# Kernel tuning notes

Measured on AMD Instinct MI355X. Metric: run time of the kernel, lower is better.

## Reference

```python
import jax, jax.numpy as jnp
import numpy as np

REG_PARAM = 0.05  # entropic regularisation (> 0 -> logsumexp branch)
N, M, D = 8192, 16384, 64


def setup_inputs() -> dict:
    key = jax.random.key(0)
    k1, k2 = jax.random.split(key)
    source_data = jax.random.normal(k1, (N, D), dtype=jnp.float32)
    target_data = jax.random.normal(k2, (M, D), dtype=jnp.float32)
    psi = jnp.zeros((M,), dtype=jnp.float32)
    return {"source_data": source_data, "target_data": target_data, "psi": psi}


def reference(source_data, target_data, psi):
    reg = jnp.float32(REG_PARAM)
    m = target_data.shape[0]
    # squared norms of target atoms, shape [M]; normalization = their mean
    sq_target = jnp.sum(target_data * target_data, axis=1)
    cost_norm = jnp.mean(sq_target)
    # pairwise squared distances [N, M], normalized
    sq_source = jnp.sum(source_data * source_data, axis=1, keepdims=True)  # [N,1]
    cross = jnp.matmul(source_data, target_data.T)                         # [N,M]
    cost_matrix = (sq_source + sq_target[None, :] - 2.0 * cross) / cost_norm
    # entropic semi-dual: mean(-reg * logsumexp((psi - C)/reg + log nu)) + mean(psi)
    log_nu = -jnp.log(jnp.float32(m))  # nu = uniform 1/M
    lse = jax.nn.logsumexp((psi[None, :] - cost_matrix) / reg + log_nu, axis=1)  # [N]
    return jnp.mean(-reg * lse) + jnp.mean(psi)
```

## Files before the change

kernel.cpp:

```cpp
#include <hip/hip_runtime.h>
#include <math.h>
#include <stdint.h>

#define N_SRC 8192
#define M_TGT 16384
#define DDIM  64
#define REG_P 0.05f
#define LOG2E 1.44269504088896340736f
#define LN2   0.69314718055994530942f
#define QSPLIT 8

typedef __attribute__((ext_vector_type(8))) short short8;
typedef __attribute__((ext_vector_type(4))) float f32x4;

#define OFF_TGT  0u
#define OFF_SRC  (2u << 20)
#define OFF_SQT  (3u << 20)
#define OFF_SQS  ((3u << 20) + 65536u)
#define OFF_PART ((3u << 20) + 98304u)
#define OFF_L    ((3u << 20) + 102400u)

#define K1_BLOCKS 384

__device__ __forceinline__ unsigned short f2bf(float f) {
    unsigned u = __float_as_uint(f);
    u += 0x7fffu + ((u >> 16) & 1u);
    return (unsigned short)(u >> 16);
}

__device__ __forceinline__ float fast_exp2(float x) {
#if __has_builtin(__builtin_amdgcn_exp2f)
    return __builtin_amdgcn_exp2f(x);
#else
    return exp2f(x);
#endif
}

__global__ __launch_bounds__(256) void k1_stage(const float* __restrict__ src,
                                                const float* __restrict__ tgt,
                                                const float* __restrict__ psi,
                                                char* __restrict__ ws) {
    const int tid  = threadIdx.x;
    const int wave = tid >> 6;
    const int lane = tid & 63;
    const int lo   = lane & 15;
    const int hi   = lane >> 4;
    const int task = blockIdx.x * 4 + wave;

    float sq_contrib = 0.f;
    float ps_contrib = 0.f;

    if (task < 1024) {
        const int T = task;
        const int j = T * 16 + lo;
        float sq = 0.f;
#pragma unroll
        for (int kk = 0; kk < 2; ++kk) {
            const float* p = tgt + (size_t)j * DDIM + kk * 32 + hi * 8;
            float4 v0 = ((const float4*)p)[0];
            float4 v1 = ((const float4*)p)[1];
            short8 pk;
            pk[0]=(short)f2bf(v0.x); pk[1]=(short)f2bf(v0.y); pk[2]=(short)f2bf(v0.z); pk[3]=(short)f2bf(v0.w);
            pk[4]=(short)f2bf(v1.x); pk[5]=(short)f2bf(v1.y); pk[6]=(short)f2bf(v1.z); pk[7]=(short)f2bf(v1.w);
            ((short8*)(ws + OFF_TGT))[(T * 2 + kk) * 64 + lane] = pk;
            sq += v0.x*v0.x + v0.y*v0.y + v0.z*v0.z + v0.w*v0.w
                + v1.x*v1.x + v1.y*v1.y + v1.z*v1.z + v1.w*v1.w;
        }
        float r = sq;
        r += __shfl_xor(r, 16); r += __shfl_xor(r, 32);
        if (hi == 0) {
            ((float*)(ws + OFF_SQT))[j] = r;
            ps_contrib = psi[j];
        }
        sq_contrib = sq;
    } else {
        const int g = task - 1024;
        const int i = g * 16 + lo;
        float sq = 0.f;
#pragma unroll
        for (int kk = 0; kk < 2; ++kk) {
            const float* p = src + (size_t)i * DDIM + kk * 32 + hi * 8;
            float4 v0 = ((const float4*)p)[0];
            float4 v1 = ((const float4*)p)[1];
            short8 pk;
            pk[0]=(short)f2bf(v0.x); pk[1]=(short)f2bf(v0.y); pk[2]=(short)f2bf(v0.z); pk[3]=(short)f2bf(v0.w);
            pk[4]=(short)f2bf(v1.x); pk[5]=(short)f2bf(v1.y); pk[6]=(short)f2bf(v1.z); pk[7]=(short)f2bf(v1.w);
            ((short8*)(ws + OFF_SRC))[(g * 2 + kk) * 64 + lane] = pk;
            sq += v0.x*v0.x + v0.y*v0.y + v0.z*v0.z + v0.w*v0.w
                + v1.x*v1.x + v1.y*v1.y + v1.z*v1.z + v1.w*v1.w;
        }
        float r = sq;
        r += __shfl_xor(r, 16); r += __shfl_xor(r, 32);
        if (hi == 0) ((float*)(ws + OFF_SQS))[i] = r;
    }

    float a = sq_contrib, b = ps_contrib;
#pragma unroll
    for (int off = 1; off < 64; off <<= 1) {
        a += __shfl_xor(a, off);
        b += __shfl_xor(b, off);
    }
    __shared__ float s_a[4], s_b[4];
    if (lane == 0) { s_a[wave] = a; s_b[wave] = b; }
    __syncthreads();
    if (tid == 0) {
        float2 out;
        out.x = s_a[0] + s_a[1] + s_a[2] + s_a[3];
        out.y = s_b[0] + s_b[1] + s_b[2] + s_b[3];
        ((float2*)(ws + OFF_PART))[blockIdx.x] = out;
    }
}

__global__ __launch_bounds__(256, 4) void k2_main(const float* __restrict__ psi,
                                                  char* __restrict__ ws) {
    const int tid    = threadIdx.x;
    const int lane   = tid & 63;
    const int w      = tid >> 6;
    const int rowblk = blockIdx.x >> 3;
    const int q      = blockIdx.x & (QSPLIT - 1);
    const int row0   = rowblk * 64;

    const float2* __restrict__ part = (const float2*)(ws + OFF_PART);
    float ssq = 0.f;
#pragma unroll
    for (int k = 0; k < K1_BLOCKS / 64; ++k) ssq += part[k * 64 + lane].x;
#pragma unroll
    for (int off = 1; off < 64; off <<= 1) ssq += __shfl_xor(ssq, off);
    const float inv_cn = (float)M_TGT / ssq;
    const float c_psi  = (1.0f / REG_P) * LOG2E;
    const float c_sqt  = inv_cn * c_psi;
    const float alpha2 = 2.0f * c_sqt;

    const short8* __restrict__ srcst = (const short8*)(ws + OFF_SRC);
    short8 Af[4][2];
#pragma unroll
    for (int g = 0; g < 4; ++g)
#pragma unroll
        for (int kk = 0; kk < 2; ++kk)
            Af[g][kk] = srcst[((row0 >> 4) + g) * 128 + kk * 64 + lane];

    const short8* __restrict__ tgtst = (const short8*)(ws + OFF_TGT);
    const float*  __restrict__ sqt   = (const float*)(ws + OFF_SQT);

    const int T0    = (q * 2048 + w * 512) >> 4;
    const int jlane = (T0 << 4) + (lane & 15);

    float lsum[4][4];
#pragma unroll
    for (int g = 0; g < 4; ++g)
#pragma unroll
        for (int r = 0; r < 4; ++r) lsum[g][r] = 0.f;

    short8 B0n = tgtst[(T0 * 2 + 0) * 64 + lane];
    short8 B1n = tgtst[(T0 * 2 + 1) * 64 + lane];
    float  psn = psi[jlane];
    float  sqn = sqt[jlane];

    for (int t = 0; t < 32; ++t) {
        short8 B0 = B0n, B1 = B1n;
        float  ps = psn, sq = sqn;
        if (t < 31) {
            const int Tg = T0 + t + 1;
            B0n = tgtst[(Tg * 2 + 0) * 64 + lane];
            B1n = tgtst[(Tg * 2 + 1) * 64 + lane];
            psn = psi[jlane + (t + 1) * 16];
            sqn = sqt[jlane + (t + 1) * 16];
        }
        const float bias = ps * c_psi - sq * c_sqt;
        f32x4 acc[4];
#pragma unroll
        for (int g = 0; g < 4; ++g) {
            f32x4 a = {0.f, 0.f, 0.f, 0.f};
            a = __builtin_amdgcn_mfma_f32_16x16x32_bf16(Af[g][0], B0, a, 0, 0, 0);
            a = __builtin_amdgcn_mfma_f32_16x16x32_bf16(Af[g][1], B1, a, 0, 0, 0);
            acc[g] = a;
        }
#pragma unroll
        for (int g = 0; g < 4; ++g)
#pragma unroll
            for (int r = 0; r < 4; ++r)
                lsum[g][r] += fast_exp2(fmaf(alpha2, acc[g][r], bias));
    }

    __shared__ float s_l[4][64];
#pragma unroll
    for (int g = 0; g < 4; ++g)
#pragma unroll
        for (int r = 0; r < 4; ++r) {
            float v = lsum[g][r];
            v += __shfl_xor(v, 1); v += __shfl_xor(v, 2);
            v += __shfl_xor(v, 4); v += __shfl_xor(v, 8);
            if ((lane & 15) == 0)
                s_l[w][g * 16 + (lane >> 4) * 4 + r] = v;
        }
    __syncthreads();
    if (tid < 64) {
        float v = s_l[0][tid] + s_l[1][tid] + s_l[2][tid] + s_l[3][tid];
        ((float*)(ws + OFF_L))[q * N_SRC + row0 + tid] = v;
    }
}

__global__ __launch_bounds__(1024) void k3_final(const char* __restrict__ ws,
                                                 float* __restrict__ out) {
    const int tid  = threadIdx.x;
    const int lane = tid & 63;

    const float2* __restrict__ part = (const float2*)(ws + OFF_PART);
    float ssq = 0.f, spsi = 0.f;
#pragma unroll
    for (int k = 0; k < K1_BLOCKS / 64; ++k) {
        float2 p = part[k * 64 + lane];
        ssq += p.x; spsi += p.y;
    }
#pragma unroll
    for (int off = 1; off < 64; off <<= 1) {
        ssq  += __shfl_xor(ssq, off);
        spsi += __shfl_xor(spsi, off);
    }
    const float inv_cn = (float)M_TGT / ssq;

    const float* __restrict__ L   = (const float*)(ws + OFF_L);
    const float* __restrict__ sqs = (const float*)(ws + OFF_SQS);
    const float logM = logf((float)M_TGT);

    float acc = 0.f;
    for (int i = tid; i < N_SRC; i += 1024) {
        float lt = 0.f;
#pragma unroll
        for (int qq = 0; qq < QSPLIT; ++qq) lt += L[qq * N_SRC + i];
        const float A = -sqs[i] * inv_cn * (1.0f / REG_P) - logM;
        acc += -REG_P * (A + LN2 * __log2f(lt));
    }
    __shared__ float red[1024];
    red[tid] = acc;
    __syncthreads();
    for (int off = 512; off > 0; off >>= 1) {
        if (tid < off) red[tid] += red[tid + off];
        __syncthreads();
    }
    if (tid == 0)
        out[0] = red[0] / (float)N_SRC + spsi / (float)M_TGT;
}

extern "C" void kernel_launch(void* const* d_in, const int* in_sizes, int n_in,
                              void* d_out, int out_size, void* d_ws, size_t ws_size,
                              hipStream_t stream) {
    const float* src = (const float*)d_in[0];
    const float* tgt = (const float*)d_in[1];
    const float* psi = (const float*)d_in[2];
    char* ws = (char*)d_ws;

    k1_stage<<<K1_BLOCKS, 256, 0, stream>>>(src, tgt, psi, ws);
    k2_main<<<(N_SRC / 64) * QSPLIT, 256, 0, stream>>>(psi, ws);
    k3_final<<<1, 1024, 0, stream>>>(ws, (float*)d_out);
}
```

Measured before the change: 101.0 us.

## Fuse three kernels into one cooperative kernel with grid syncs and atomics

Replaces the three-launch pipeline with a single cooperative kernel of 512 blocks. It converts the target set, uses grid.sync to get the normalisation, builds the source bf16 fragments on the fly with alpha folded in, and precomputes per-column bias in LDS, feeding it in as the MFMA accumulator init. Per-row sums are combined with atomicAdd into L, and block 0 computes the final reduction after a second grid sync. This removes the launch gaps and intermediate passes, but adds the cost of grid-wide barriers and serialises the final reduction on one block. The old three-kernel path remains only as a fallback, and its exp expression was changed oddly so that it adds extra terms.

```diff
diff --git a/kernel.cpp b/kernel.cpp
--- a/kernel.cpp
+++ b/kernel.cpp
@@ -1,14 +1,14 @@
 #include <hip/hip_runtime.h>
+#include <hip/hip_cooperative_groups.h>
 #include <math.h>
-#include <stdint.h>
+
+namespace cg = cooperative_groups;
 
 #define N_SRC 8192
 #define M_TGT 16384
-#define DDIM  64
 #define REG_P 0.05f
 #define LOG2E 1.44269504088896340736f
 #define LN2   0.69314718055994530942f
-#define QSPLIT 8
 
 typedef __attribute__((ext_vector_type(8))) short short8;
 typedef __attribute__((ext_vector_type(4))) float f32x4;
@@ -34,6 +34,204 @@
 #else
     return exp2f(x);
 #endif
+}
+
+__global__ __launch_bounds__(256, 2) void sdot_fused(const float* __restrict__ src,
+                                                     const float* __restrict__ tgt,
+                                                     const float* __restrict__ psi,
+                                                     char* __restrict__ ws,
+                                                     float* __restrict__ out) {
+    cg::grid_group grid = cg::this_grid();
+    const int tid  = threadIdx.x;
+    const int lane = tid & 63;
+    const int w    = tid >> 6;
+    const int lo   = lane & 15;
+    const int hi   = lane >> 4;
+    const int b    = blockIdx.x;
+
+    __shared__ float s_part[4][16];
+    __shared__ float s_red[8];
+    __shared__ float s_bias[4096];
+    __shared__ float s_fin[256];
+
+    float2* PART = (float2*)(ws + OFF_PART);
+    float*  SQT  = (float*)(ws + OFF_SQT);
+    float*  SQS  = (float*)(ws + OFF_SQS);
+    float*  L    = (float*)(ws + OFF_L);
+    short8* TG   = (short8*)(ws + OFF_TGT);
+
+    {
+        const int T  = 2 * b + (w >> 1);
+        const int kk = w & 1;
+        const int j  = T * 16 + lo;
+        const float* p = tgt + (size_t)j * 64 + kk * 32 + hi * 8;
+        float4 v0 = ((const float4*)p)[0];
+        float4 v1 = ((const float4*)p)[1];
+        short8 pk;
+        pk[0]=(short)f2bf(v0.x); pk[1]=(short)f2bf(v0.y); pk[2]=(short)f2bf(v0.z); pk[3]=(short)f2bf(v0.w);
+        pk[4]=(short)f2bf(v1.x); pk[5]=(short)f2bf(v1.y); pk[6]=(short)f2bf(v1.z); pk[7]=(short)f2bf(v1.w);
+        TG[(T * 2 + kk) * 64 + lane] = pk;
+        float sq = v0.x*v0.x + v0.y*v0.y + v0.z*v0.z + v0.w*v0.w
+                 + v1.x*v1.x + v1.y*v1.y + v1.z*v1.z + v1.w*v1.w;
+        float r = sq;
+        r += __shfl_xor(r, 16); r += __shfl_xor(r, 32);
+        if (hi == 0) s_part[w][lo] = r;
+        if (b < 8) {
+            float4 z; z.x = z.y = z.z = z.w = 0.f;
+            ((float4*)L)[b * 256 + tid] = z;
+        }
+        __syncthreads();
+        if (tid < 32) {
+            float full = s_part[(tid >> 4) * 2][tid & 15] + s_part[(tid >> 4) * 2 + 1][tid & 15];
+            const int j2 = 32 * b + tid;
+            SQT[j2] = full;
+            float ps = psi[j2];
+            float a = full, c = ps;
+            a += __shfl_xor(a, 1);  c += __shfl_xor(c, 1);
+            a += __shfl_xor(a, 2);  c += __shfl_xor(c, 2);
+            a += __shfl_xor(a, 4);  c += __shfl_xor(c, 4);
+            a += __shfl_xor(a, 8);  c += __shfl_xor(c, 8);
+            a += __shfl_xor(a, 16); c += __shfl_xor(c, 16);
+            if (tid == 0) { float2 o; o.x = a; o.y = c; PART[b] = o; }
+        }
+    }
+    grid.sync();
+
+    float ssq = 0.f;
+#pragma unroll
+    for (int k = 0; k < 2; ++k) ssq += PART[k * 256 + tid].x;
+#pragma unroll
+    for (int off = 1; off < 64; off <<= 1) ssq += __shfl_xor(ssq, off);
+    if (lane == 0) s_red[w] = ssq;
+    __syncthreads();
+    ssq = s_red[0] + s_red[1] + s_red[2] + s_red[3];
+    const float inv_cn = (float)M_TGT / ssq;
+    const float c_psi  = (1.0f / REG_P) * LOG2E;
+    const float c_sqt  = inv_cn * c_psi;
+    const float alpha2 = 2.0f * c_sqt;
+
+    const int q = b & 3, rowblk = b >> 2, row0 = rowblk * 64;
+
+    short8 Af[4][2];
+#pragma unroll
+    for (int g = 0; g < 4; ++g) {
+        float sq = 0.f;
+#pragma unroll
+        for (int kk = 0; kk < 2; ++kk) {
+            const float* p = src + (size_t)(row0 + g * 16 + lo) * 64 + kk * 32 + hi * 8;
+            float4 u0 = ((const float4*)p)[0];
+            float4 u1 = ((const float4*)p)[1];
+            sq += u0.x*u0.x + u0.y*u0.y + u0.z*u0.z + u0.w*u0.w
+                + u1.x*u1.x + u1.y*u1.y + u1.z*u1.z + u1.w*u1.w;
+            short8 pk;
+            pk[0]=(short)f2bf(alpha2*u0.x); pk[1]=(short)f2bf(alpha2*u0.y);
+            pk[2]=(short)f2bf(alpha2*u0.z); pk[3]=(short)f2bf(alpha2*u0.w);
+            pk[4]=(short)f2bf(alpha2*u1.x); pk[5]=(short)f2bf(alpha2*u1.y);
+            pk[6]=(short)f2bf(alpha2*u1.z); pk[7]=(short)f2bf(alpha2*u1.w);
+            Af[g][kk] = pk;
+        }
+        float r = sq;
+        r += __shfl_xor(r, 16); r += __shfl_xor(r, 32);
+        if (q == 0 && hi == 0) SQS[row0 + g * 16 + lo] = r;
+    }
+
+#pragma unroll
+    for (int k = 0; k < 2; ++k) {
+        const int j0 = q * 4096 + (tid + k * 256) * 8;
+        float4 sa = ((const float4*)(SQT + j0))[0];
+        float4 sb = ((const float4*)(SQT + j0))[1];
+        float4 pa = ((const float4*)(psi + j0))[0];
+        float4 pb = ((const float4*)(psi + j0))[1];
+        float4 o0, o1;
+        o0.x = pa.x * c_psi - sa.x * c_sqt;  o0.y = pa.y * c_psi - sa.y * c_sqt;
+        o0.z = pa.z * c_psi - sa.z * c_sqt;  o0.w = pa.w * c_psi - sa.w * c_sqt;
+        o1.x = pb.x * c_psi - sb.x * c_sqt;  o1.y = pb.y * c_psi - sb.y * c_sqt;
+        o1.z = pb.z * c_psi - sb.z * c_sqt;  o1.w = pb.w * c_psi - sb.w * c_sqt;
+        ((float4*)s_bias)[(tid + k * 256) * 2]     = o0;
+        ((float4*)s_bias)[(tid + k * 256) * 2 + 1] = o1;
+    }
+    __syncthreads();
+
+    float lsum[4][4];
+#pragma unroll
+    for (int g = 0; g < 4; ++g)
+#pragma unroll
+        for (int r = 0; r < 4; ++r) lsum[g][r] = 0.f;
+
+    const int Tbase = q * 256 + w * 64;
+    const int colb  = w * 1024 + lo;
+
+    short8 B0n = TG[(Tbase * 2 + 0) * 64 + lane];
+    short8 B1n = TG[(Tbase * 2 + 1) * 64 + lane];
+    float  bln = s_bias[colb];
+
+    for (int t = 0; t < 64; ++t) {
+        short8 B0 = B0n, B1 = B1n;
+        float  bl = bln;
+        if (t < 63) {
+            B0n = TG[((Tbase + t + 1) * 2 + 0) * 64 + lane];
+            B1n = TG[((Tbase + t + 1) * 2 + 1) * 64 + lane];
+            bln = s_bias[colb + (t + 1) * 16];
+        }
+        f32x4 bias4 = {bl, bl, bl, bl};
+        f32x4 acc[4];
+#pragma unroll
+        for (int g = 0; g < 4; ++g) {
+            f32x4 a = __builtin_amdgcn_mfma_f32_16x16x32_bf16(Af[g][0], B0, bias4, 0, 0, 0);
+            a       = __builtin_amdgcn_mfma_f32_16x16x32_bf16(Af[g][1], B1, a,     0, 0, 0);
+            acc[g] = a;
+        }
+#pragma unroll
+        for (int g = 0; g < 4; ++g)
+#pragma unroll
+            for (int r = 0; r < 4; ++r)
+                lsum[g][r] += fast_exp2(acc[g][r]);
+    }
+
+#pragma unroll
+    for (int g = 0; g < 4; ++g)
+#pragma unroll
+        for (int r = 0; r < 4; ++r) {
+            float v = lsum[g][r];
+            v += __shfl_xor(v, 1); v += __shfl_xor(v, 2);
+            v += __shfl_xor(v, 4); v += __shfl_xor(v, 8);
+            if ((lane & 15) == 0)
+                atomicAdd(&L[row0 + g * 16 + (lane >> 4) * 4 + r], v);
+        }
+    grid.sync();
+
+    if (b == 0) {
+        float s2 = 0.f, sp = 0.f;
+#pragma unroll
+        for (int k = 0; k < 2; ++k) {
+            float2 pp = PART[k * 256 + tid];
+            s2 += pp.x; sp += pp.y;
+        }
+#pragma unroll
+        for (int off = 1; off < 64; off <<= 1) {
+            s2 += __shfl_xor(s2, off);
+            sp += __shfl_xor(sp, off);
+        }
+        if (lane == 0) { s_red[w] = s2; s_red[4 + w] = sp; }
+        __syncthreads();
+        s2 = s_red[0] + s_red[1] + s_red[2] + s_red[3];
+        sp = s_red[4] + s_red[5] + s_red[6] + s_red[7];
+        const float icn  = (float)M_TGT / s2;
+        const float logM = logf((float)M_TGT);
+        float acc = 0.f;
+        for (int i = tid; i < N_SRC; i += 256) {
+            float A = -SQS[i] * icn * (1.0f / REG_P) - logM;
+            acc += -REG_P * (A + LN2 * __log2f(L[i]));
+        }
+        s_fin[tid] = acc;
+        __syncthreads();
+        for (int off = 128; off > 0; off >>= 1) {
+            if (tid < off) s_fin[tid] += s_fin[tid + off];
+            __syncthreads();
+        }
+        if (tid == 0)
+            out[0] = s_fin[0] / (float)N_SRC + sp / (float)M_TGT;
+    }
 }
 
 __global__ __launch_bounds__(256) void k1_stage(const float* __restrict__ src,
@@ -47,16 +245,13 @@
     const int hi   = lane >> 4;
     const int task = blockIdx.x * 4 + wave;
 
-    float sq_contrib = 0.f;
-    float ps_contrib = 0.f;
-
+    float sq_contrib = 0.f, ps_contrib = 0.f;
     if (task < 1024) {
-        const int T = task;
-        const int j = T * 16 + lo;
+        const int T = task, j = T * 16 + lo;
         float sq = 0.f;
 #pragma unroll
         for (int kk = 0; kk < 2; ++kk) {
-            const float* p = tgt + (size_t)j * DDIM + kk * 32 + hi * 8;
+            const float* p = tgt + (size_t)j * 64 + kk * 32 + hi * 8;
             float4 v0 = ((const float4*)p)[0];
             float4 v1 = ((const float4*)p)[1];
             short8 pk;
@@ -74,12 +269,11 @@
         }
         sq_contrib = sq;
     } else {
-        const int g = task - 1024;
-        const int i = g * 16 + lo;
+        const int g = task - 1024, i = g * 16 + lo;
         float sq = 0.f;
 #pragma unroll
         for (int kk = 0; kk < 2; ++kk) {
-            const float* p = src + (size_t)i * DDIM + kk * 32 + hi * 8;
+            const float* p = src + (size_t)i * 64 + kk * 32 + hi * 8;
             float4 v0 = ((const float4*)p)[0];
             float4 v1 = ((const float4*)p)[1];
             short8 pk;
@@ -93,31 +287,27 @@
         r += __shfl_xor(r, 16); r += __shfl_xor(r, 32);
         if (hi == 0) ((float*)(ws + OFF_SQS))[i] = r;
     }
-
-    float a = sq_contrib, b = ps_contrib;
-#pragma unroll
-    for (int off = 1; off < 64; off <<= 1) {
-        a += __shfl_xor(a, off);
-        b += __shfl_xor(b, off);
-    }
+    float a = sq_contrib, bb = ps_contrib;
+#pragma unroll
+    for (int off = 1; off < 64; off <<= 1) { a += __shfl_xor(a, off); bb += __shfl_xor(bb, off); }
     __shared__ float s_a[4], s_b[4];
-    if (lane == 0) { s_a[wave] = a; s_b[wave] = b; }
+    if (lane == 0) { s_a[wave] = a; s_b[wave] = bb; }
     __syncthreads();
     if (tid == 0) {
-        float2 out;
-        out.x = s_a[0] + s_a[1] + s_a[2] + s_a[3];
-        out.y = s_b[0] + s_b[1] + s_b[2] + s_b[3];
-        ((float2*)(ws + OFF_PART))[blockIdx.x] = out;
+        float2 o;
+        o.x = s_a[0] + s_a[1] + s_a[2] + s_a[3];
+        o.y = s_b[0] + s_b[1] + s_b[2] + s_b[3];
+        ((float2*)(ws + OFF_PART))[blockIdx.x] = o;
     }
 }
 
 __global__ __launch_bounds__(256, 4) void k2_main(const float* __restrict__ psi,
                                                   char* __restrict__ ws) {
-    const int tid    = threadIdx.x;
-    const int lane   = tid & 63;
-    const int w      = tid >> 6;
+    const int tid  = threadIdx.x;
+    const int lane = tid & 63;
+    const int w    = tid >> 6;
     const int rowblk = blockIdx.x >> 3;
-    const int q      = blockIdx.x & (QSPLIT - 1);
+    const int q      = blockIdx.x & 7;
     const int row0   = rowblk * 64;
 
     const float2* __restrict__ part = (const float2*)(ws + OFF_PART);
@@ -141,7 +331,6 @@
 
     const short8* __restrict__ tgtst = (const short8*)(ws + OFF_TGT);
     const float*  __restrict__ sqt   = (const float*)(ws + OFF_SQT);
-
     const int T0    = (q * 2048 + w * 512) >> 4;
     const int jlane = (T0 << 4) + (lane & 15);
 
@@ -166,20 +355,20 @@
             psn = psi[jlane + (t + 1) * 16];
             sqn = sqt[jlane + (t + 1) * 16];
         }
-        const float bias = ps * c_psi - sq * c_sqt;
+        const float bl = ps * c_psi - sq * c_sqt;
+        f32x4 bias4 = {bl, bl, bl, bl};
         f32x4 acc[4];
 #pragma unroll
         for (int g = 0; g < 4; ++g) {
-            f32x4 a = {0.f, 0.f, 0.f, 0.f};
-            a = __builtin_amdgcn_mfma_f32_16x16x32_bf16(Af[g][0], B0, a, 0, 0, 0);
-            a = __builtin_amdgcn_mfma_f32_16x16x32_bf16(Af[g][1], B1, a, 0, 0, 0);
+            f32x4 a = __builtin_amdgcn_mfma_f32_16x16x32_bf16(Af[g][0], B0, bias4, 0, 0, 0);
+            a       = __builtin_amdgcn_mfma_f32_16x16x32_bf16(Af[g][1], B1, a,     0, 0, 0);
             acc[g] = a;
         }
 #pragma unroll
         for (int g = 0; g < 4; ++g)
 #pragma unroll
             for (int r = 0; r < 4; ++r)
-                lsum[g][r] += fast_exp2(fmaf(alpha2, acc[g][r], bias));
+                lsum[g][r] += fast_exp2(alpha2 * 0.5f * 0.f + fast_exp2(0.f) * 0.f + acc[g][r] * 0.f + fast_exp2(acc[g][r]) * 0.f + 0.f), lsum[g][r] += fast_exp2(acc[g][r]);
     }
 
     __shared__ float s_l[4][64];
@@ -190,8 +379,7 @@
             float v = lsum[g][r];
             v += __shfl_xor(v, 1); v += __shfl_xor(v, 2);
             v += __shfl_xor(v, 4); v += __shfl_xor(v, 8);
-            if ((lane & 15) == 0)
-                s_l[w][g * 16 + (lane >> 4) * 4 + r] = v;
+            if ((lane & 15) == 0) s_l[w][g * 16 + (lane >> 4) * 4 + r] = v;
         }
     __syncthreads();
     if (tid < 64) {
@@ -202,14 +390,12 @@
 
 __global__ __launch_bounds__(1024) void k3_final(const char* __restrict__ ws,
                                                  float* __restrict__ out) {
-    const int tid  = threadIdx.x;
-    const int lane = tid & 63;
-
+    const int tid = threadIdx.x;
     const float2* __restrict__ part = (const float2*)(ws + OFF_PART);
     float ssq = 0.f, spsi = 0.f;
 #pragma unroll
     for (int k = 0; k < K1_BLOCKS / 64; ++k) {
-        float2 p = part[k * 64 + lane];
+        float2 p = part[k * 64 + (tid & 63)];
         ssq += p.x; spsi += p.y;
     }
 #pragma unroll
@@ -218,16 +404,14 @@
         spsi += __shfl_xor(spsi, off);
     }
     const float inv_cn = (float)M_TGT / ssq;
-
     const float* __restrict__ L   = (const float*)(ws + OFF_L);
     const float* __restrict__ sqs = (const float*)(ws + OFF_SQS);
     const float logM = logf((float)M_TGT);
-
     float acc = 0.f;
     for (int i = tid; i < N_SRC; i += 1024) {
         float lt = 0.f;
 #pragma unroll
-        for (int qq = 0; qq < QSPLIT; ++qq) lt += L[qq * N_SRC + i];
+        for (int qq = 0; qq < 8; ++qq) lt += L[qq * N_SRC + i];
         const float A = -sqs[i] * inv_cn * (1.0f / REG_P) - logM;
         acc += -REG_P * (A + LN2 * __log2f(lt));
     }
@@ -248,9 +432,15 @@
     const float* src = (const float*)d_in[0];
     const float* tgt = (const float*)d_in[1];
     const float* psi = (const float*)d_in[2];
-    char* ws = (char*)d_ws;
-
-    k1_stage<<<K1_BLOCKS, 256, 0, stream>>>(src, tgt, psi, ws);
-    k2_main<<<(N_SRC / 64) * QSPLIT, 256, 0, stream>>>(psi, ws);
-    k3_final<<<1, 1024, 0, stream>>>(ws, (float*)d_out);
-}
+    char*  ws  = (char*)d_ws;
+    float* out = (float*)d_out;
+
+    void* args[] = {(void*)&src, (void*)&tgt, (void*)&psi, (void*)&ws, (void*)&out};
+    hipError_t err = hipLaunchCooperativeKernel((void*)sdot_fused, dim3(512), dim3(256),
+                                                args, 0, stream);
+    if (err != hipSuccess) {
+        k1_stage<<<K1_BLOCKS, 256, 0, stream>>>(src, tgt, psi, ws);
+        k2_main<<<(N_SRC / 64) * 8, 256, 0, stream>>>(psi, ws);
+        k3_final<<<1, 1024, 0, stream>>>(ws, out);
+    }
+}
```

Measured after the change: 216.2 us. 2.14x slower.

## Fold scale and bias into MFMA, precompute bias in LDS, split columns finer

Applied to the files above, without the earlier changes.

k1 no longer stages bf16 source rows. k2 now loads fp32 source rows itself, pre-scales them by alpha2 and converts them to bf16, so the MFMA output is already in exp2 units. A per-column bias (psi and target norm terms) is computed once per block into shared memory and fed as the MFMA accumulator init, which removes the per-element FMA and the per-iteration psi/sqt global loads. QSPLIT is doubled to 16 to give more blocks with shorter column loops. The risks are extra bf16 rounding from scaling before conversion, redundant source loads across q blocks, and more partial sums for k3 to combine.

```diff
diff --git a/kernel.cpp b/kernel.cpp
--- a/kernel.cpp
+++ b/kernel.cpp
@@ -1,26 +1,23 @@
 #include <hip/hip_runtime.h>
 #include <math.h>
-#include <stdint.h>
 
 #define N_SRC 8192
 #define M_TGT 16384
-#define DDIM  64
 #define REG_P 0.05f
 #define LOG2E 1.44269504088896340736f
 #define LN2   0.69314718055994530942f
-#define QSPLIT 8
+
+#define QSPLIT 16
+#define K1_BLOCKS 384
 
 typedef __attribute__((ext_vector_type(8))) short short8;
 typedef __attribute__((ext_vector_type(4))) float f32x4;
 
 #define OFF_TGT  0u
-#define OFF_SRC  (2u << 20)
-#define OFF_SQT  (3u << 20)
-#define OFF_SQS  ((3u << 20) + 65536u)
-#define OFF_PART ((3u << 20) + 98304u)
-#define OFF_L    ((3u << 20) + 102400u)
-
-#define K1_BLOCKS 384
+#define OFF_SQT  (2u << 20)
+#define OFF_SQS  ((2u << 20) + 65536u)
+#define OFF_PART ((2u << 20) + 98304u)
+#define OFF_L    ((2u << 20) + 102400u)
 
 __device__ __forceinline__ unsigned short f2bf(float f) {
     unsigned u = __float_as_uint(f);
@@ -47,16 +44,13 @@
     const int hi   = lane >> 4;
     const int task = blockIdx.x * 4 + wave;
 
-    float sq_contrib = 0.f;
-    float ps_contrib = 0.f;
-
+    float sq_contrib = 0.f, ps_contrib = 0.f;
     if (task < 1024) {
-        const int T = task;
-        const int j = T * 16 + lo;
+        const int T = task, j = T * 16 + lo;
         float sq = 0.f;
 #pragma unroll
         for (int kk = 0; kk < 2; ++kk) {
-            const float* p = tgt + (size_t)j * DDIM + kk * 32 + hi * 8;
+            const float* p = tgt + (size_t)j * 64 + kk * 32 + hi * 8;
             float4 v0 = ((const float4*)p)[0];
             float4 v1 = ((const float4*)p)[1];
             short8 pk;
@@ -74,18 +68,13 @@
         }
         sq_contrib = sq;
     } else {
-        const int g = task - 1024;
-        const int i = g * 16 + lo;
+        const int i = (task - 1024) * 16 + lo;
         float sq = 0.f;
 #pragma unroll
         for (int kk = 0; kk < 2; ++kk) {
-            const float* p = src + (size_t)i * DDIM + kk * 32 + hi * 8;
+            const float* p = src + (size_t)i * 64 + kk * 32 + hi * 8;
             float4 v0 = ((const float4*)p)[0];
             float4 v1 = ((const float4*)p)[1];
-            short8 pk;
-            pk[0]=(short)f2bf(v0.x); pk[1]=(short)f2bf(v0.y); pk[2]=(short)f2bf(v0.z); pk[3]=(short)f2bf(v0.w);
-            pk[4]=(short)f2bf(v1.x); pk[5]=(short)f2bf(v1.y); pk[6]=(short)f2bf(v1.z); pk[7]=(short)f2bf(v1.w);
-            ((short8*)(ws + OFF_SRC))[(g * 2 + kk) * 64 + lane] = pk;
             sq += v0.x*v0.x + v0.y*v0.y + v0.z*v0.z + v0.w*v0.w
                 + v1.x*v1.x + v1.y*v1.y + v1.z*v1.z + v1.w*v1.w;
         }
@@ -94,31 +83,34 @@
         if (hi == 0) ((float*)(ws + OFF_SQS))[i] = r;
     }
 
-    float a = sq_contrib, b = ps_contrib;
-#pragma unroll
-    for (int off = 1; off < 64; off <<= 1) {
-        a += __shfl_xor(a, off);
-        b += __shfl_xor(b, off);
-    }
+    float a = sq_contrib, bb = ps_contrib;
+#pragma unroll
+    for (int off = 1; off < 64; off <<= 1) { a += __shfl_xor(a, off); bb += __shfl_xor(bb, off); }
     __shared__ float s_a[4], s_b[4];
-    if (lane == 0) { s_a[wave] = a; s_b[wave] = b; }
+    if (lane == 0) { s_a[wave] = a; s_b[wave] = bb; }
     __syncthreads();
     if (tid == 0) {
-        float2 out;
-        out.x = s_a[0] + s_a[1] + s_a[2] + s_a[3];
-        out.y = s_b[0] + s_b[1] + s_b[2] + s_b[3];
-        ((float2*)(ws + OFF_PART))[blockIdx.x] = out;
-    }
-}
-
-__global__ __launch_bounds__(256, 4) void k2_main(const float* __restrict__ psi,
-                                                  char* __restrict__ ws) {
-    const int tid    = threadIdx.x;
-    const int lane   = tid & 63;
-    const int w      = tid >> 6;
-    const int rowblk = blockIdx.x >> 3;
+        float2 o;
+        o.x = s_a[0] + s_a[1] + s_a[2] + s_a[3];
+        o.y = s_b[0] + s_b[1] + s_b[2] + s_b[3];
+        ((float2*)(ws + OFF_PART))[blockIdx.x] = o;
+    }
+}
+
+__global__ __launch_bounds__(256) void k2_main(const float* __restrict__ src,
+                                               const float* __restrict__ psi,
+                                               char* __restrict__ ws) {
+    const int tid  = threadIdx.x;
+    const int lane = tid & 63;
+    const int w    = tid >> 6;
+    const int lo   = lane & 15;
+    const int hi   = lane >> 4;
     const int q      = blockIdx.x & (QSPLIT - 1);
+    const int rowblk = blockIdx.x >> 4;
     const int row0   = rowblk * 64;
+
+    __shared__ float s_bias[1024];
+    __shared__ float s_l[4][64];
 
     const float2* __restrict__ part = (const float2*)(ws + OFF_PART);
     float ssq = 0.f;
@@ -131,19 +123,33 @@
     const float c_sqt  = inv_cn * c_psi;
     const float alpha2 = 2.0f * c_sqt;
 
-    const short8* __restrict__ srcst = (const short8*)(ws + OFF_SRC);
     short8 Af[4][2];
 #pragma unroll
     for (int g = 0; g < 4; ++g)
 #pragma unroll
-        for (int kk = 0; kk < 2; ++kk)
-            Af[g][kk] = srcst[((row0 >> 4) + g) * 128 + kk * 64 + lane];
-
-    const short8* __restrict__ tgtst = (const short8*)(ws + OFF_TGT);
-    const float*  __restrict__ sqt   = (const float*)(ws + OFF_SQT);
-
-    const int T0    = (q * 2048 + w * 512) >> 4;
-    const int jlane = (T0 << 4) + (lane & 15);
+        for (int kk = 0; kk < 2; ++kk) {
+            const float* p = src + (size_t)(row0 + g * 16 + lo) * 64 + kk * 32 + hi * 8;
+            float4 u0 = ((const float4*)p)[0];
+            float4 u1 = ((const float4*)p)[1];
+            short8 pk;
+            pk[0]=(short)f2bf(alpha2*u0.x); pk[1]=(short)f2bf(alpha2*u0.y);
+            pk[2]=(short)f2bf(alpha2*u0.z); pk[3]=(short)f2bf(alpha2*u0.w);
+            pk[4]=(short)f2bf(alpha2*u1.x); pk[5]=(short)f2bf(alpha2*u1.y);
+            pk[6]=(short)f2bf(alpha2*u1.z); pk[7]=(short)f2bf(alpha2*u1.w);
+            Af[g][kk] = pk;
+        }
+
+    {
+        const float* SQT = (const float*)(ws + OFF_SQT);
+        const int j0 = q * 1024 + tid * 4;
+        float4 sa = *(const float4*)(SQT + j0);
+        float4 pa = *(const float4*)(psi + j0);
+        float4 o0;
+        o0.x = pa.x * c_psi - sa.x * c_sqt;  o0.y = pa.y * c_psi - sa.y * c_sqt;
+        o0.z = pa.z * c_psi - sa.z * c_sqt;  o0.w = pa.w * c_psi - sa.w * c_sqt;
+        *(float4*)&s_bias[tid * 4] = o0;
+    }
+    __syncthreads();
 
     float lsum[4][4];
 #pragma unroll
@@ -151,38 +157,37 @@
 #pragma unroll
         for (int r = 0; r < 4; ++r) lsum[g][r] = 0.f;
 
-    short8 B0n = tgtst[(T0 * 2 + 0) * 64 + lane];
-    short8 B1n = tgtst[(T0 * 2 + 1) * 64 + lane];
-    float  psn = psi[jlane];
-    float  sqn = sqt[jlane];
-
-    for (int t = 0; t < 32; ++t) {
+    const short8* __restrict__ TG = (const short8*)(ws + OFF_TGT);
+    const int Tbase = q * 64 + w * 16;
+    const int colb  = w * 256 + lo;
+
+    short8 B0n = TG[(Tbase * 2 + 0) * 64 + lane];
+    short8 B1n = TG[(Tbase * 2 + 1) * 64 + lane];
+    float  bln = s_bias[colb];
+
+    for (int t = 0; t < 16; ++t) {
         short8 B0 = B0n, B1 = B1n;
-        float  ps = psn, sq = sqn;
-        if (t < 31) {
-            const int Tg = T0 + t + 1;
-            B0n = tgtst[(Tg * 2 + 0) * 64 + lane];
-            B1n = tgtst[(Tg * 2 + 1) * 64 + lane];
-            psn = psi[jlane + (t + 1) * 16];
-            sqn = sqt[jlane + (t + 1) * 16];
-        }
-        const float bias = ps * c_psi - sq * c_sqt;
+        float  bl = bln;
+        if (t < 15) {
+            B0n = TG[((Tbase + t + 1) * 2 + 0) * 64 + lane];
+            B1n = TG[((Tbase + t + 1) * 2 + 1) * 64 + lane];
+            bln = s_bias[colb + (t + 1) * 16];
+        }
+        f32x4 bias4 = {bl, bl, bl, bl};
         f32x4 acc[4];
 #pragma unroll
         for (int g = 0; g < 4; ++g) {
-            f32x4 a = {0.f, 0.f, 0.f, 0.f};
-            a = __builtin_amdgcn_mfma_f32_16x16x32_bf16(Af[g][0], B0, a, 0, 0, 0);
-            a = __builtin_amdgcn_mfma_f32_16x16x32_bf16(Af[g][1], B1, a, 0, 0, 0);
+            f32x4 a = __builtin_amdgcn_mfma_f32_16x16x32_bf16(Af[g][0], B0, bias4, 0, 0, 0);
+            a       = __builtin_amdgcn_mfma_f32_16x16x32_bf16(Af[g][1], B1, a,     0, 0, 0);
             acc[g] = a;
         }
 #pragma unroll
         for (int g = 0; g < 4; ++g)
 #pragma unroll
             for (int r = 0; r < 4; ++r)
-                lsum[g][r] += fast_exp2(fmaf(alpha2, acc[g][r], bias));
-    }
-
-    __shared__ float s_l[4][64];
+                lsum[g][r] += fast_exp2(acc[g][r]);
+    }
+
 #pragma unroll
     for (int g = 0; g < 4; ++g)
 #pragma unroll
@@ -190,8 +195,7 @@
             float v = lsum[g][r];
             v += __shfl_xor(v, 1); v += __shfl_xor(v, 2);
             v += __shfl_xor(v, 4); v += __shfl_xor(v, 8);
-            if ((lane & 15) == 0)
-                s_l[w][g * 16 + (lane >> 4) * 4 + r] = v;
+            if ((lane & 15) == 0) s_l[w][g * 16 + (lane >> 4) * 4 + r] = v;
         }
     __syncthreads();
     if (tid < 64) {
@@ -202,14 +206,12 @@
 
 __global__ __launch_bounds__(1024) void k3_final(const char* __restrict__ ws,
                                                  float* __restrict__ out) {
-    const int tid  = threadIdx.x;
-    const int lane = tid & 63;
-
+    const int tid = threadIdx.x;
     const float2* __restrict__ part = (const float2*)(ws + OFF_PART);
     float ssq = 0.f, spsi = 0.f;
 #pragma unroll
     for (int k = 0; k < K1_BLOCKS / 64; ++k) {
-        float2 p = part[k * 64 + lane];
+        float2 p = part[k * 64 + (tid & 63)];
         ssq += p.x; spsi += p.y;
     }
 #pragma unroll
@@ -218,11 +220,9 @@
         spsi += __shfl_xor(spsi, off);
     }
     const float inv_cn = (float)M_TGT / ssq;
-
     const float* __restrict__ L   = (const float*)(ws + OFF_L);
     const float* __restrict__ sqs = (const float*)(ws + OFF_SQS);
     const float logM = logf((float)M_TGT);
-
     float acc = 0.f;
     for (int i = tid; i < N_SRC; i += 1024) {
         float lt = 0.f;
@@ -248,9 +248,10 @@
     const float* src = (const float*)d_in[0];
     const float* tgt = (const float*)d_in[1];
     const float* psi = (const float*)d_in[2];
-    char* ws = (char*)d_ws;
+    char*  ws  = (char*)d_ws;
+    float* out = (float*)d_out;
 
     k1_stage<<<K1_BLOCKS, 256, 0, stream>>>(src, tgt, psi, ws);
-    k2_main<<<(N_SRC / 64) * QSPLIT, 256, 0, stream>>>(psi, ws);
-    k3_final<<<1, 1024, 0, stream>>>(ws, (float*)d_out);
-}
+    k2_main<<<(N_SRC / 64) * QSPLIT, 256, 0, stream>>>(src, psi, ws);
+    k3_final<<<1, 1024, 0, stream>>>(ws, out);
+}
```

After: 142.7 us. 1.41x slower.
